# Kernel optimization log

Hardware: AMD Instinct MI355X
Metric: run time of the kernel (lower is better)

## Reference

```python
import jax, jax.numpy as jnp
import numpy as np

N_NODES = 10000
N_EDGES = 160000
BATCH = 16
F_IN = 32          # NODE_EMBED_SIZE
HEADS = 4
HDIM = 4
HC = HEADS * HDIM  # 16
N_LAYERS = 4
OBS_DIM = 100
NUM_OUT = 30
HID = 128
POOL_OUT = 15


def setup_inputs() -> dict:
    key = jax.random.key(0)
    ks = jax.random.split(key, 26)
    s = 0.1
    d = {}
    d["x"] = jax.random.normal(ks[0], (BATCH, N_NODES, F_IN), jnp.float32)
    d["obs"] = jax.random.normal(ks[1], (BATCH, OBS_DIM), jnp.float32)
    d["src"] = jax.random.randint(ks[2], (N_EDGES,), 0, N_NODES)
    d["dst"] = jax.random.randint(ks[3], (N_EDGES,), 0, N_NODES)
    # layer 0 (in=F_IN), layers 1..3 (in=HC) GATv2 params
    d["W0l"] = jax.random.normal(ks[4], (F_IN, HC)) * s
    d["W0r"] = jax.random.normal(ks[5], (F_IN, HC)) * s
    d["b0l"] = jnp.zeros((HC,), jnp.float32)
    d["b0r"] = jnp.zeros((HC,), jnp.float32)
    d["Wl"] = jax.random.normal(ks[6], (N_LAYERS - 1, HC, HC)) * s
    d["Wr"] = jax.random.normal(ks[7], (N_LAYERS - 1, HC, HC)) * s
    d["bl"] = jnp.zeros((N_LAYERS - 1, HC), jnp.float32)
    d["br"] = jnp.zeros((N_LAYERS - 1, HC), jnp.float32)
    d["att"] = jax.random.normal(ks[8], (N_LAYERS, HEADS, HDIM)) * s
    d["bias"] = jnp.zeros((N_LAYERS, HC), jnp.float32)
    # mean-pool aggregator projection to 15
    d["Wp"] = jax.random.normal(ks[9], (HC, POOL_OUT)) * s
    d["bp"] = jnp.zeros((POOL_OUT,), jnp.float32)
    # hybrid policy head: cat([feat15, obs100]) -> 128 -> 128 -> num_outputs
    d["W1"] = jax.random.normal(ks[10], (POOL_OUT + OBS_DIM, HID)) * s
    d["b1"] = jnp.zeros((HID,), jnp.float32)
    d["W2"] = jax.random.normal(ks[11], (HID, HID)) * s
    d["b2"] = jnp.zeros((HID,), jnp.float32)
    d["W3"] = jax.random.normal(ks[12], (HID, NUM_OUT)) * s
    d["b3"] = jnp.zeros((NUM_OUT,), jnp.float32)
    return d


def _gatv2_layer(x, src, dst, Wl, Wr, bl, br, att, bias):
    # x: [B,N,F]; src/dst: [E'] (self loops included); att: [H,C]
    B, N, _ = x.shape
    H, C = att.shape
    xl = (x @ Wl + bl).reshape(B, N, H, C)  # source transform
    xr = (x @ Wr + br).reshape(B, N, H, C)  # target transform
    z = jax.nn.leaky_relu(xl[:, src] + xr[:, dst], negative_slope=0.2)  # [B,E,H,C]
    e = jnp.einsum('behc,hc->ebh', z, att)  # [E,B,H] edge-major for segment ops
    m = jax.lax.stop_gradient(jax.ops.segment_max(e, dst, num_segments=N))
    m = jnp.where(jnp.isfinite(m), m, 0.0)
    ex = jnp.exp(e - m[dst])
    ssum = jax.ops.segment_sum(ex, dst, num_segments=N)
    alpha = ex / (ssum[dst] + 1e-16)  # softmax over incoming edges of dst
    msg = xl[:, src] * jnp.transpose(alpha, (1, 0, 2))[..., None]  # [B,E,H,C]
    out = jax.ops.segment_sum(jnp.transpose(msg, (1, 0, 2, 3)), dst, num_segments=N)
    return jnp.transpose(out, (1, 0, 2, 3)).reshape(B, N, H * C) + bias


def reference(x, obs, src, dst, W0l, W0r, b0l, b0r, Wl, Wr, bl, br, att, bias,
              Wp, bp, W1, b1, W2, b2, W3, b3):
    N = x.shape[1]
    loop = jnp.arange(N, dtype=src.dtype)  # PyG add_self_loops=True
    src_f = jnp.concatenate([src, loop])
    dst_f = jnp.concatenate([dst, loop])
    h = _gatv2_layer(x, src_f, dst_f, W0l, W0r, b0l, b0r, att[0], bias[0])
    for l in range(N_LAYERS - 1):
        h = _gatv2_layer(h, src_f, dst_f, Wl[l], Wr[l], bl[l], br[l], att[l + 1], bias[l + 1])
    feat = h.mean(axis=1) @ Wp + bp  # mean-pool aggregator -> [B,15]
    z1 = jnp.tanh(jnp.concatenate([feat, obs], axis=1) @ W1 + b1)
    z2 = jnp.tanh(z1 @ W2 + b2)
    return z2 @ W3 + b3  # logits [B, NUM_OUT]
```

## Files before the change

### kernel.cpp

```cpp
#include <hip/hip_runtime.h>
#include <hip/hip_fp16.h>
#include <cstdint>
#include <cstddef>

#define NN   10000
#define NE   160000
#define NB   16
#define FIN  32
#define HC   16
#define NH   4
#define HD   4
#define OBSD 100
#define NOUT 30
#define HIDD 128
#define PO   15
#define BCAP 64
#define NBUCKET 64

typedef float floatx2 __attribute__((ext_vector_type(2)));

__device__ inline uint32_t pack_fp8x4(float a, float b, float c, float d) {
    int p = __builtin_amdgcn_cvt_pk_fp8_f32(a, b, 0, false);
    p = __builtin_amdgcn_cvt_pk_fp8_f32(c, d, p, true);
    return (uint32_t)p;
}

__global__ void k_build_xform0(const int* __restrict__ src, const int* __restrict__ dst,
                               int* __restrict__ cnt, int* __restrict__ bucket,
                               const float* __restrict__ x,
                               const float* __restrict__ Wlg, const float* __restrict__ Wrg,
                               const float* __restrict__ blg, const float* __restrict__ brg,
                               uint32_t* __restrict__ xl, float* __restrict__ xr) {
    int bid = blockIdx.x;
    if (bid < 625) {
        int e = bid * 256 + threadIdx.x;
        if (e < NE) {
            int d = dst[e];
            int p = atomicAdd(&cnt[d], 1);
            if (p < BCAP) bucket[(size_t)d * BCAP + p] = src[e];
        }
        return;
    }
    __shared__ float sWl[FIN * HC], sWr[FIN * HC], sbl[HC], sbr[HC];
    for (int i = threadIdx.x; i < FIN * HC; i += 256) { sWl[i] = Wlg[i]; sWr[i] = Wrg[i]; }
    if (threadIdx.x < HC) { sbl[threadIdx.x] = blg[threadIdx.x]; sbr[threadIdx.x] = brg[threadIdx.x]; }
    __syncthreads();
    int local = bid - 625;
    int b = local / 40;
    int n = (local % 40) * 256 + threadIdx.x;
    if (n >= NN) return;
    const float* xp = x + ((size_t)b * NN + n) * FIN;
    float row[FIN];
#pragma unroll
    for (int f = 0; f < FIN; f++) row[f] = xp[f];
    float al[HC], ar[HC];
#pragma unroll
    for (int c = 0; c < HC; c++) { al[c] = sbl[c]; ar[c] = sbr[c]; }
#pragma unroll
    for (int f = 0; f < FIN; f++) {
        float v = row[f];
#pragma unroll
        for (int c = 0; c < HC; c++) {
            al[c] = fmaf(v, sWl[f * HC + c], al[c]);
            ar[c] = fmaf(v, sWr[f * HC + c], ar[c]);
        }
    }
    uint32_t* xlo = xl + ((size_t)n * NB + b) * 4;
    float*    xro = xr + ((size_t)n * NB + b) * HC;
#pragma unroll
    for (int hh = 0; hh < 4; hh++)
        xlo[hh] = pack_fp8x4(al[hh * 4 + 0], al[hh * 4 + 1], al[hh * 4 + 2], al[hh * 4 + 3]);
#pragma unroll
    for (int c = 0; c < HC; c++) xro[c] = ar[c];
}

__device__ inline float4 shfl_xor4(float4 v, int m) {
    float4 r;
    r.x = __shfl_xor(v.x, m, 64);
    r.y = __shfl_xor(v.y, m, 64);
    r.z = __shfl_xor(v.z, m, 64);
    r.w = __shfl_xor(v.w, m, 64);
    return r;
}

template <int MODE>
__global__ __launch_bounds__(256, 4)
void k_edge_f(const uint32_t* __restrict__ xl, const float* __restrict__ xr,
              const int* __restrict__ cntg, const int* __restrict__ bucket,
              const float* __restrict__ attg, const float* __restrict__ biasg,
              const float* __restrict__ Wln, const float* __restrict__ Wrn,
              const float* __restrict__ bln, const float* __restrict__ brn,
              uint32_t* __restrict__ xl_o, float* __restrict__ xr_o,
              float* __restrict__ pool_part) {
    __shared__ float sWl[HC * HC], sWr[HC * HC], sbl[HC], sbr[HC];
    if (MODE == 1) {
        int t = threadIdx.x;
        sWl[t] = Wln[t]; sWr[t] = Wrn[t];
        if (t < HC) { sbl[t] = bln[t]; sbr[t] = brn[t]; }
        __syncthreads();
    }
    int wave = (blockIdx.x * blockDim.x + threadIdx.x) >> 6;
    int lane = threadIdx.x & 63;
    const int n = wave;
    const int h = lane & 3;
    const float4 a4 = *(const float4*)(attg + h * HD);
    const float4 bias4 = *(const float4*)(biasg + h * HD);
    const float4 xr4 = *(const float4*)(xr + (size_t)n * (NB * HC) + lane * 4);
    const int cnt = __builtin_amdgcn_readfirstlane(cntg[n]);
    float4 acc = make_float4(0.f, 0.f, 0.f, 0.f);
    float ssum = 0.f;

#define EDGE_BODY(RAW, M)                                                     \
    {                                                                         \
        floatx2 f0 = __builtin_amdgcn_cvt_pk_f32_fp8((int)(RAW), false);      \
        floatx2 f1 = __builtin_amdgcn_cvt_pk_f32_fp8((int)(RAW), true);       \
        float z0 = f0.x + xr4.x; z0 = fmaxf(z0, 0.2f * z0);                   \
        float z1 = f0.y + xr4.y; z1 = fmaxf(z1, 0.2f * z1);                   \
        float z2 = f1.x + xr4.z; z2 = fmaxf(z2, 0.2f * z2);                   \
        float z3 = f1.y + xr4.w; z3 = fmaxf(z3, 0.2f * z3);                   \
        float e = fmaf(z3, a4.w, fmaf(z2, a4.z, fmaf(z1, a4.y, z0 * a4.x)));  \
        float ex = (M) * __expf(e);                                           \
        ssum += ex;                                                           \
        acc.x = fmaf(ex, f0.x, acc.x);                                        \
        acc.y = fmaf(ex, f0.y, acc.y);                                        \
        acc.z = fmaf(ex, f1.x, acc.z);                                        \
        acc.w = fmaf(ex, f1.y, acc.w);                                        \
    }
#define GATHER(S) xl[(size_t)(S) * 64 + lane]

    {
        const uint32_t r = GATHER(n);
        EDGE_BODY(r, 1.0f);
    }
    if (cnt > 0) {
        const int* brow = bucket + (size_t)n * BCAP;
        int li = lane < cnt ? lane : cnt - 1;
        int vidx = brow[li];
        for (int i = 0; i < cnt; i += 16) {
            uint32_t r[16];
#pragma unroll
            for (int u = 0; u < 16; u++) {
                int e = i + u;
                int ec = e < cnt ? e : cnt - 1;
                int s = __builtin_amdgcn_readlane(vidx, ec);
                r[u] = GATHER(s);
            }
#pragma unroll
            for (int u = 0; u < 16; u++) {
                float m = (i + u < cnt) ? 1.0f : 0.0f;
                EDGE_BODY(r[u], m);
            }
        }
    }
#undef GATHER
#undef EDGE_BODY

    float inv = 1.0f / (ssum + 1e-16f);
    float4 o;
    o.x = fmaf(acc.x, inv, bias4.x);
    o.y = fmaf(acc.y, inv, bias4.y);
    o.z = fmaf(acc.z, inv, bias4.z);
    o.w = fmaf(acc.w, inv, bias4.w);

    if (MODE == 1) {
        float accl[4], accr[4];
#pragma unroll
        for (int cj = 0; cj < 4; cj++) {
            accl[cj] = sbl[h * 4 + cj];
            accr[cj] = sbr[h * 4 + cj];
        }
#pragma unroll
        for (int m = 0; m < 4; m++) {
            float4 vals = (m == 0) ? o : shfl_xor4(o, m);
            int fbase = ((h ^ m) << 2);
            float vv[4] = {vals.x, vals.y, vals.z, vals.w};
#pragma unroll
            for (int j = 0; j < 4; j++) {
                const float4 wl = *(const float4*)&sWl[(fbase + j) * HC + (h << 2)];
                const float4 wr = *(const float4*)&sWr[(fbase + j) * HC + (h << 2)];
                float v = vv[j];
                accl[0] = fmaf(v, wl.x, accl[0]);
                accl[1] = fmaf(v, wl.y, accl[1]);
                accl[2] = fmaf(v, wl.z, accl[2]);
                accl[3] = fmaf(v, wl.w, accl[3]);
                accr[0] = fmaf(v, wr.x, accr[0]);
                accr[1] = fmaf(v, wr.y, accr[1]);
                accr[2] = fmaf(v, wr.z, accr[2]);
                accr[3] = fmaf(v, wr.w, accr[3]);
            }
        }
        xl_o[(size_t)n * 64 + lane] = pack_fp8x4(accl[0], accl[1], accl[2], accl[3]);
        *(float4*)(xr_o + (size_t)n * (NB * HC) + lane * 4) =
            make_float4(accr[0], accr[1], accr[2], accr[3]);
    } else {
        __shared__ float sRed[256 * 4];
        int tid = threadIdx.x;
        *(float4*)&sRed[tid * 4] = o;
        __syncthreads();
        if (tid < 64) {
            float4 s0 = *(const float4*)&sRed[tid * 4];
            float4 s1 = *(const float4*)&sRed[(64 + tid) * 4];
            float4 s2 = *(const float4*)&sRed[(128 + tid) * 4];
            float4 s3 = *(const float4*)&sRed[(192 + tid) * 4];
            float* dp = pool_part + (blockIdx.x & (NBUCKET - 1)) * 256 + tid * 4;
            atomicAdd(dp + 0, s0.x + s1.x + s2.x + s3.x);
            atomicAdd(dp + 1, s0.y + s1.y + s2.y + s3.y);
            atomicAdd(dp + 2, s0.z + s1.z + s2.z + s3.z);
            atomicAdd(dp + 3, s0.w + s1.w + s2.w + s3.w);
        }
    }
}

__global__ void k_head(const float* __restrict__ pool_part, const float* __restrict__ obs,
                       const float* __restrict__ Wp, const float* __restrict__ bp,
                       const float* __restrict__ W1, const float* __restrict__ b1,
                       const float* __restrict__ W2, const float* __restrict__ b2,
                       const float* __restrict__ W3, const float* __restrict__ b3,
                       float* __restrict__ out) {
    const int b = blockIdx.x;
    const int t = threadIdx.x;
    __shared__ float sPool[HC];
    __shared__ float sIn[PO + OBSD];
    __shared__ float s1[HIDD], s2[HIDD];
    if (t < HC) {
        float ps = 0.f;
        for (int p = 0; p < NBUCKET; p++) ps += pool_part[p * 256 + b * HC + t];
        sPool[t] = ps * (1.0f / NN);
    }
    for (int k = t; k < OBSD; k += 128) sIn[PO + k] = obs[b * OBSD + k];
    __syncthreads();
    if (t < PO) {
        float acc = bp[t];
#pragma unroll
        for (int c = 0; c < HC; c++) acc = fmaf(sPool[c], Wp[c * PO + t], acc);
        sIn[t] = acc;
    }
    __syncthreads();
    {
        float acc = b1[t];
        for (int k = 0; k < PO + OBSD; k++) acc = fmaf(sIn[k], W1[k * HIDD + t], acc);
        s1[t] = tanhf(acc);
    }
    __syncthreads();
    {
        float acc = b2[t];
        for (int k = 0; k < HIDD; k++) acc = fmaf(s1[k], W2[k * HIDD + t], acc);
        s2[t] = tanhf(acc);
    }
    __syncthreads();
    if (t < NOUT) {
        float acc = b3[t];
        for (int k = 0; k < HIDD; k++) acc = fmaf(s2[k], W3[k * NOUT + t], acc);
        out[b * NOUT + t] = acc;
    }
}

extern "C" void kernel_launch(void* const* d_in, const int* in_sizes, int n_in,
                              void* d_out, int out_size, void* d_ws, size_t ws_size,
                              hipStream_t stream) {
    const float* x    = (const float*)d_in[0];
    const float* obs  = (const float*)d_in[1];
    const int*   src  = (const int*)d_in[2];
    const int*   dst  = (const int*)d_in[3];
    const float* W0l  = (const float*)d_in[4];
    const float* W0r  = (const float*)d_in[5];
    const float* b0l  = (const float*)d_in[6];
    const float* b0r  = (const float*)d_in[7];
    const float* Wl   = (const float*)d_in[8];
    const float* Wr   = (const float*)d_in[9];
    const float* bl   = (const float*)d_in[10];
    const float* br   = (const float*)d_in[11];
    const float* att  = (const float*)d_in[12];
    const float* bias = (const float*)d_in[13];
    const float* Wp   = (const float*)d_in[14];
    const float* bp   = (const float*)d_in[15];
    const float* W1   = (const float*)d_in[16];
    const float* b1   = (const float*)d_in[17];
    const float* W2   = (const float*)d_in[18];
    const float* b2   = (const float*)d_in[19];
    const float* W3   = (const float*)d_in[20];
    const float* b3   = (const float*)d_in[21];
    float* out = (float*)d_out;

    size_t off = 0;
    auto take = [&](size_t bytes) -> void* {
        void* p = (char*)d_ws + off;
        off += (bytes + 255) & ~(size_t)255;
        return p;
    };
    int*      cnt       = (int*)take(NN * sizeof(int));
    float*    pool_part = (float*)take(NBUCKET * 256 * sizeof(float));
    int*      bucket    = (int*)take((size_t)NN * BCAP * sizeof(int));
    uint32_t* xlA       = (uint32_t*)take((size_t)NN * 64 * sizeof(uint32_t));
    float*    xrA       = (float*)take((size_t)NN * NB * HC * sizeof(float));
    uint32_t* xlB       = (uint32_t*)take((size_t)NN * 64 * sizeof(uint32_t));
    float*    xrB       = (float*)take((size_t)NN * NB * HC * sizeof(float));

    size_t zspan = (size_t)((char*)(pool_part + NBUCKET * 256) - (char*)cnt);
    hipMemsetAsync(cnt, 0, zspan, stream);

    k_build_xform0<<<625 + 40 * NB, 256, 0, stream>>>(src, dst, cnt, bucket,
                                                      x, W0l, W0r, b0l, b0r, xlA, xrA);

    const int EG = (NN * 64) / 256;
    k_edge_f<1><<<EG, 256, 0, stream>>>(xlA, xrA, cnt, bucket,
                                        att + 0 * 16, bias + 0 * 16,
                                        Wl + 0 * 256, Wr + 0 * 256, bl + 0 * 16, br + 0 * 16,
                                        xlB, xrB, nullptr);
    k_edge_f<1><<<EG, 256, 0, stream>>>(xlB, xrB, cnt, bucket,
                                        att + 1 * 16, bias + 1 * 16,
                                        Wl + 1 * 256, Wr + 1 * 256, bl + 1 * 16, br + 1 * 16,
                                        xlA, xrA, nullptr);
    k_edge_f<1><<<EG, 256, 0, stream>>>(xlA, xrA, cnt, bucket,
                                        att + 2 * 16, bias + 2 * 16,
                                        Wl + 2 * 256, Wr + 2 * 256, bl + 2 * 16, br + 2 * 16,
                                        xlB, xrB, nullptr);
    k_edge_f<2><<<EG, 256, 0, stream>>>(xlB, xrB, cnt, bucket,
                                        att + 3 * 16, bias + 3 * 16,
                                        nullptr, nullptr, nullptr, nullptr,
                                        nullptr, nullptr, pool_part);

    k_head<<<NB, HIDD, 0, stream>>>(pool_part, obs, Wp, bp, W1, b1, W2, b2, W3, b3, out);
}
```

Baseline: 131.3 us.

## Store xr in fp16 and fuse policy head into last edge kernel

The xr target-transform buffers change from fp32 to fp16, halving their write and read traffic in every layer. The separate k_head launch is removed: the last edge kernel counts finished blocks with an atomic, and the last block reduces the pool partials and runs the MLP head for all 16 batches itself. The number of pool-partial buckets is halved and the bucket count is clamped to BCAP. This trades one launch and some memory traffic for fp16 precision loss and a head computed serially by a single block.

```diff
diff --git a/kernel.cpp b/kernel.cpp
--- a/kernel.cpp
+++ b/kernel.cpp
@@ -15,7 +15,8 @@
 #define HIDD 128
 #define PO   15
 #define BCAP 64
-#define NBUCKET 64
+#define NBUCKET 32
+#define EG   2500
 
 typedef float floatx2 __attribute__((ext_vector_type(2)));
 
@@ -23,6 +24,15 @@
     int p = __builtin_amdgcn_cvt_pk_fp8_f32(a, b, 0, false);
     p = __builtin_amdgcn_cvt_pk_fp8_f32(c, d, p, true);
     return (uint32_t)p;
+}
+
+__device__ inline float4 shfl_xor4(float4 v, int m) {
+    float4 r;
+    r.x = __shfl_xor(v.x, m, 64);
+    r.y = __shfl_xor(v.y, m, 64);
+    r.z = __shfl_xor(v.z, m, 64);
+    r.w = __shfl_xor(v.w, m, 64);
+    return r;
 }
 
 __global__ void k_build_xform0(const int* __restrict__ src, const int* __restrict__ dst,
@@ -30,7 +40,7 @@
                                const float* __restrict__ x,
                                const float* __restrict__ Wlg, const float* __restrict__ Wrg,
                                const float* __restrict__ blg, const float* __restrict__ brg,
-                               uint32_t* __restrict__ xl, float* __restrict__ xr) {
+                               uint32_t* __restrict__ xl, __half* __restrict__ xr) {
     int bid = blockIdx.x;
     if (bid < 625) {
         int e = bid * 256 + threadIdx.x;
@@ -66,47 +76,53 @@
         }
     }
     uint32_t* xlo = xl + ((size_t)n * NB + b) * 4;
-    float*    xro = xr + ((size_t)n * NB + b) * HC;
+    __half2*  xro = (__half2*)(xr + ((size_t)n * NB + b) * HC);
 #pragma unroll
     for (int hh = 0; hh < 4; hh++)
         xlo[hh] = pack_fp8x4(al[hh * 4 + 0], al[hh * 4 + 1], al[hh * 4 + 2], al[hh * 4 + 3]);
 #pragma unroll
-    for (int c = 0; c < HC; c++) xro[c] = ar[c];
-}
-
-__device__ inline float4 shfl_xor4(float4 v, int m) {
-    float4 r;
-    r.x = __shfl_xor(v.x, m, 64);
-    r.y = __shfl_xor(v.y, m, 64);
-    r.z = __shfl_xor(v.z, m, 64);
-    r.w = __shfl_xor(v.w, m, 64);
-    return r;
+    for (int c = 0; c < HC; c += 2) xro[c >> 1] = __floats2half2_rn(ar[c], ar[c + 1]);
 }
 
 template <int MODE>
 __global__ __launch_bounds__(256, 4)
-void k_edge_f(const uint32_t* __restrict__ xl, const float* __restrict__ xr,
+void k_edge_f(const uint32_t* __restrict__ xl, const __half* __restrict__ xr,
               const int* __restrict__ cntg, const int* __restrict__ bucket,
               const float* __restrict__ attg, const float* __restrict__ biasg,
               const float* __restrict__ Wln, const float* __restrict__ Wrn,
               const float* __restrict__ bln, const float* __restrict__ brn,
-              uint32_t* __restrict__ xl_o, float* __restrict__ xr_o,
-              float* __restrict__ pool_part) {
-    __shared__ float sWl[HC * HC], sWr[HC * HC], sbl[HC], sbr[HC];
+              uint32_t* __restrict__ xl_o, __half* __restrict__ xr_o,
+              float* __restrict__ pool_part, int* __restrict__ done,
+              const float* __restrict__ obs,
+              const float* __restrict__ Wp, const float* __restrict__ bp,
+              const float* __restrict__ W1, const float* __restrict__ b1,
+              const float* __restrict__ W2, const float* __restrict__ b2,
+              const float* __restrict__ W3, const float* __restrict__ b3,
+              float* __restrict__ out) {
+    __shared__ float smem[MODE == 2 ? 6208 : 544];
     if (MODE == 1) {
         int t = threadIdx.x;
-        sWl[t] = Wln[t]; sWr[t] = Wrn[t];
-        if (t < HC) { sbl[t] = bln[t]; sbr[t] = brn[t]; }
-        __syncthreads();
-    }
-    int wave = (blockIdx.x * blockDim.x + threadIdx.x) >> 6;
-    int lane = threadIdx.x & 63;
+        smem[t] = Wln[t];
+        smem[256 + t] = Wrn[t];
+        if (t < HC) { smem[512 + t] = bln[t]; smem[528 + t] = brn[t]; }
+        __syncthreads();
+    }
+    const int tid  = threadIdx.x;
+    const int wave = (blockIdx.x * 256 + tid) >> 6;
+    const int lane = tid & 63;
     const int n = wave;
     const int h = lane & 3;
     const float4 a4 = *(const float4*)(attg + h * HD);
     const float4 bias4 = *(const float4*)(biasg + h * HD);
-    const float4 xr4 = *(const float4*)(xr + (size_t)n * (NB * HC) + lane * 4);
-    const int cnt = __builtin_amdgcn_readfirstlane(cntg[n]);
+    float4 xr4;
+    {
+        const uint2 xrr = *(const uint2*)(xr + (size_t)n * (NB * HC) + lane * 4);
+        float2 p0 = __half22float2(*(const __half2*)&xrr.x);
+        float2 p1 = __half22float2(*(const __half2*)&xrr.y);
+        xr4 = make_float4(p0.x, p0.y, p1.x, p1.y);
+    }
+    int cnt = __builtin_amdgcn_readfirstlane(cntg[n]);
+    cnt = cnt < BCAP ? cnt : BCAP;
     float4 acc = make_float4(0.f, 0.f, 0.f, 0.f);
     float ssum = 0.f;
 
@@ -128,10 +144,7 @@
     }
 #define GATHER(S) xl[(size_t)(S) * 64 + lane]
 
-    {
-        const uint32_t r = GATHER(n);
-        EDGE_BODY(r, 1.0f);
-    }
+    { const uint32_t r = GATHER(n); EDGE_BODY(r, 1.0f); }
     if (cnt > 0) {
         const int* brow = bucket + (size_t)n * BCAP;
         int li = lane < cnt ? lane : cnt - 1;
@@ -166,8 +179,8 @@
         float accl[4], accr[4];
 #pragma unroll
         for (int cj = 0; cj < 4; cj++) {
-            accl[cj] = sbl[h * 4 + cj];
-            accr[cj] = sbr[h * 4 + cj];
+            accl[cj] = smem[512 + h * 4 + cj];
+            accr[cj] = smem[528 + h * 4 + cj];
         }
 #pragma unroll
         for (int m = 0; m < 4; m++) {
@@ -176,8 +189,8 @@
             float vv[4] = {vals.x, vals.y, vals.z, vals.w};
 #pragma unroll
             for (int j = 0; j < 4; j++) {
-                const float4 wl = *(const float4*)&sWl[(fbase + j) * HC + (h << 2)];
-                const float4 wr = *(const float4*)&sWr[(fbase + j) * HC + (h << 2)];
+                const float4 wl = *(const float4*)&smem[(fbase + j) * HC + (h << 2)];
+                const float4 wr = *(const float4*)&smem[256 + (fbase + j) * HC + (h << 2)];
                 float v = vv[j];
                 accl[0] = fmaf(v, wl.x, accl[0]);
                 accl[1] = fmaf(v, wl.y, accl[1]);
@@ -190,68 +203,80 @@
             }
         }
         xl_o[(size_t)n * 64 + lane] = pack_fp8x4(accl[0], accl[1], accl[2], accl[3]);
-        *(float4*)(xr_o + (size_t)n * (NB * HC) + lane * 4) =
-            make_float4(accr[0], accr[1], accr[2], accr[3]);
+        __half2* xro = (__half2*)(xr_o + (size_t)n * (NB * HC) + lane * 4);
+        xro[0] = __floats2half2_rn(accr[0], accr[1]);
+        xro[1] = __floats2half2_rn(accr[2], accr[3]);
     } else {
-        __shared__ float sRed[256 * 4];
-        int tid = threadIdx.x;
+        float* sRed = smem;
         *(float4*)&sRed[tid * 4] = o;
         __syncthreads();
         if (tid < 64) {
             float4 s0 = *(const float4*)&sRed[tid * 4];
-            float4 s1 = *(const float4*)&sRed[(64 + tid) * 4];
-            float4 s2 = *(const float4*)&sRed[(128 + tid) * 4];
-            float4 s3 = *(const float4*)&sRed[(192 + tid) * 4];
+            float4 s1v = *(const float4*)&sRed[(64 + tid) * 4];
+            float4 s2v = *(const float4*)&sRed[(128 + tid) * 4];
+            float4 s3v = *(const float4*)&sRed[(192 + tid) * 4];
             float* dp = pool_part + (blockIdx.x & (NBUCKET - 1)) * 256 + tid * 4;
-            atomicAdd(dp + 0, s0.x + s1.x + s2.x + s3.x);
-            atomicAdd(dp + 1, s0.y + s1.y + s2.y + s3.y);
-            atomicAdd(dp + 2, s0.z + s1.z + s2.z + s3.z);
-            atomicAdd(dp + 3, s0.w + s1.w + s2.w + s3.w);
-        }
-    }
-}
-
-__global__ void k_head(const float* __restrict__ pool_part, const float* __restrict__ obs,
-                       const float* __restrict__ Wp, const float* __restrict__ bp,
-                       const float* __restrict__ W1, const float* __restrict__ b1,
-                       const float* __restrict__ W2, const float* __restrict__ b2,
-                       const float* __restrict__ W3, const float* __restrict__ b3,
-                       float* __restrict__ out) {
-    const int b = blockIdx.x;
-    const int t = threadIdx.x;
-    __shared__ float sPool[HC];
-    __shared__ float sIn[PO + OBSD];
-    __shared__ float s1[HIDD], s2[HIDD];
-    if (t < HC) {
-        float ps = 0.f;
-        for (int p = 0; p < NBUCKET; p++) ps += pool_part[p * 256 + b * HC + t];
-        sPool[t] = ps * (1.0f / NN);
-    }
-    for (int k = t; k < OBSD; k += 128) sIn[PO + k] = obs[b * OBSD + k];
-    __syncthreads();
-    if (t < PO) {
-        float acc = bp[t];
-#pragma unroll
-        for (int c = 0; c < HC; c++) acc = fmaf(sPool[c], Wp[c * PO + t], acc);
-        sIn[t] = acc;
-    }
-    __syncthreads();
-    {
-        float acc = b1[t];
-        for (int k = 0; k < PO + OBSD; k++) acc = fmaf(sIn[k], W1[k * HIDD + t], acc);
-        s1[t] = tanhf(acc);
-    }
-    __syncthreads();
-    {
-        float acc = b2[t];
-        for (int k = 0; k < HIDD; k++) acc = fmaf(s1[k], W2[k * HIDD + t], acc);
-        s2[t] = tanhf(acc);
-    }
-    __syncthreads();
-    if (t < NOUT) {
-        float acc = b3[t];
-        for (int k = 0; k < HIDD; k++) acc = fmaf(s2[k], W3[k * NOUT + t], acc);
-        out[b * NOUT + t] = acc;
+            atomicAdd(dp + 0, s0.x + s1v.x + s2v.x + s3v.x);
+            atomicAdd(dp + 1, s0.y + s1v.y + s2v.y + s3v.y);
+            atomicAdd(dp + 2, s0.z + s1v.z + s2v.z + s3v.z);
+            atomicAdd(dp + 3, s0.w + s1v.w + s2v.w + s3v.w);
+        }
+        __syncthreads();
+        __shared__ int lastFlag;
+        if (tid == 0) {
+            int t = __hip_atomic_fetch_add(done, 1, __ATOMIC_ACQ_REL,
+                                           __HIP_MEMORY_SCOPE_AGENT);
+            lastFlag = (t == EG - 1) ? 1 : 0;
+        }
+        __syncthreads();
+        if (!lastFlag) return;
+
+        float* sPool = smem;
+        float* sIn   = smem + 256;
+        float* s1a   = smem + 2112;
+        float* s2a   = smem + 4160;
+        {
+            int b = tid >> 4, c = tid & 15;
+            float ps = 0.f;
+            for (int q = 0; q < NBUCKET; q++)
+                ps += __hip_atomic_load(&pool_part[q * 256 + b * HC + c],
+                                        __ATOMIC_RELAXED, __HIP_MEMORY_SCOPE_AGENT);
+            sPool[tid] = ps * (1.0f / NN);
+        }
+        __syncthreads();
+        for (int k = tid; k < NB * (PO + OBSD); k += 256) {
+            int b = k / (PO + OBSD), j = k - b * (PO + OBSD);
+            float v;
+            if (j < PO) {
+                v = bp[j];
+#pragma unroll
+                for (int c = 0; c < HC; c++) v = fmaf(sPool[b * HC + c], Wp[c * PO + j], v);
+            } else {
+                v = obs[b * OBSD + (j - PO)];
+            }
+            sIn[b * 116 + j] = v;
+        }
+        __syncthreads();
+        for (int k = tid; k < NB * HIDD; k += 256) {
+            int b = k >> 7, t = k & 127;
+            float acc2 = b1[t];
+            for (int j = 0; j < PO + OBSD; j++) acc2 = fmaf(sIn[b * 116 + j], W1[j * HIDD + t], acc2);
+            s1a[k] = tanhf(acc2);
+        }
+        __syncthreads();
+        for (int k = tid; k < NB * HIDD; k += 256) {
+            int b = k >> 7, t = k & 127;
+            float acc2 = b2[t];
+            for (int j = 0; j < HIDD; j++) acc2 = fmaf(s1a[b * 128 + j], W2[j * HIDD + t], acc2);
+            s2a[k] = tanhf(acc2);
+        }
+        __syncthreads();
+        for (int k = tid; k < NB * NOUT; k += 256) {
+            int b = k / NOUT, t = k - b * NOUT;
+            float acc2 = b3[t];
+            for (int j = 0; j < HIDD; j++) acc2 = fmaf(s2a[b * 128 + j], W3[j * NOUT + t], acc2);
+            out[k] = acc2;
+        }
     }
 }
 
@@ -284,41 +309,46 @@
 
     size_t off = 0;
     auto take = [&](size_t bytes) -> void* {
-        void* p = (char*)d_ws + off;
+        void* ptr = (char*)d_ws + off;
         off += (bytes + 255) & ~(size_t)255;
-        return p;
+        return ptr;
     };
+    int*      done      = (int*)take(64 * sizeof(int));
     int*      cnt       = (int*)take(NN * sizeof(int));
     float*    pool_part = (float*)take(NBUCKET * 256 * sizeof(float));
     int*      bucket    = (int*)take((size_t)NN * BCAP * sizeof(int));
     uint32_t* xlA       = (uint32_t*)take((size_t)NN * 64 * sizeof(uint32_t));
-    float*    xrA       = (float*)take((size_t)NN * NB * HC * sizeof(float));
+    __half*   xrA       = (__half*)take((size_t)NN * NB * HC * sizeof(__half));
     uint32_t* xlB       = (uint32_t*)take((size_t)NN * 64 * sizeof(uint32_t));
-    float*    xrB       = (float*)take((size_t)NN * NB * HC * sizeof(float));
-
-    size_t zspan = (size_t)((char*)(pool_part + NBUCKET * 256) - (char*)cnt);
-    hipMemsetAsync(cnt, 0, zspan, stream);
+    __half*   xrB       = (__half*)take((size_t)NN * NB * HC * sizeof(__half));
+
+    size_t zspan = (size_t)((char*)(pool_part + NBUCKET * 256) - (char*)done);
+    hipMemsetAsync(done, 0, zspan, stream);
 
     k_build_xform0<<<625 + 40 * NB, 256, 0, stream>>>(src, dst, cnt, bucket,
                                                       x, W0l, W0r, b0l, b0r, xlA, xrA);
 
-    const int EG = (NN * 64) / 256;
     k_edge_f<1><<<EG, 256, 0, stream>>>(xlA, xrA, cnt, bucket,
                                         att + 0 * 16, bias + 0 * 16,
                                         Wl + 0 * 256, Wr + 0 * 256, bl + 0 * 16, br + 0 * 16,
-                                        xlB, xrB, nullptr);
+                                        xlB, xrB, nullptr, nullptr,
+                                        nullptr, nullptr, nullptr, nullptr, nullptr,
+                                        nullptr, nullptr, nullptr, nullptr, nullptr);
     k_edge_f<1><<<EG, 256, 0, stream>>>(xlB, xrB, cnt, bucket,
                                         att + 1 * 16, bias + 1 * 16,
                                         Wl + 1 * 256, Wr + 1 * 256, bl + 1 * 16, br + 1 * 16,
-                                        xlA, xrA, nullptr);
+                                        xlA, xrA, nullptr, nullptr,
+                                        nullptr, nullptr, nullptr, nullptr, nullptr,
+                                        nullptr, nullptr, nullptr, nullptr, nullptr);
     k_edge_f<1><<<EG, 256, 0, stream>>>(xlA, xrA, cnt, bucket,
                                         att + 2 * 16, bias + 2 * 16,
                                         Wl + 2 * 256, Wr + 2 * 256, bl + 2 * 16, br + 2 * 16,
-                                        xlB, xrB, nullptr);
+                                        xlB, xrB, nullptr, nullptr,
+                                        nullptr, nullptr, nullptr, nullptr, nullptr,
+                                        nullptr, nullptr, nullptr, nullptr, nullptr);
     k_edge_f<2><<<EG, 256, 0, stream>>>(xlB, xrB, cnt, bucket,
                                         att + 3 * 16, bias + 3 * 16,
                                         nullptr, nullptr, nullptr, nullptr,
-                                        nullptr, nullptr, pool_part);
-
-    k_head<<<NB, HIDD, 0, stream>>>(pool_part, obs, Wp, bp, W1, b1, W2, b2, W3, b3, out);
-}
+                                        nullptr, nullptr, pool_part, done,
+                                        obs, Wp, bp, W1, b1, W2, b2, W3, b3, out);
+}
```

Result: slower. 206.2 us (+57.1%).

## Store xr in fp16 and replace pool atomics with per-block partials

Applied to the files above, without the earlier changes.

The target-side transform xr is now stored as fp16 instead of fp32, which halves its memory traffic in every edge layer and lowers precision. The final layer no longer does atomicAdd into 64 buckets; each block writes its own 256-float partial, and the head kernel, now 256 threads, reduces all 2500 partials. This removes atomic contention and the memset of the pool buffer, but adds a serial reduction inside the small head kernel. The edge count is also clamped to BCAP, and shared memory is merged into a single array.

```diff
diff --git a/kernel.cpp b/kernel.cpp
--- a/kernel.cpp
+++ b/kernel.cpp
@@ -15,7 +15,7 @@
 #define HIDD 128
 #define PO   15
 #define BCAP 64
-#define NBUCKET 64
+#define EG   2500
 
 typedef float floatx2 __attribute__((ext_vector_type(2)));
 
@@ -23,6 +23,15 @@
     int p = __builtin_amdgcn_cvt_pk_fp8_f32(a, b, 0, false);
     p = __builtin_amdgcn_cvt_pk_fp8_f32(c, d, p, true);
     return (uint32_t)p;
+}
+
+__device__ inline float4 shfl_xor4(float4 v, int m) {
+    float4 r;
+    r.x = __shfl_xor(v.x, m, 64);
+    r.y = __shfl_xor(v.y, m, 64);
+    r.z = __shfl_xor(v.z, m, 64);
+    r.w = __shfl_xor(v.w, m, 64);
+    return r;
 }
 
 __global__ void k_build_xform0(const int* __restrict__ src, const int* __restrict__ dst,
@@ -30,7 +39,7 @@
                                const float* __restrict__ x,
                                const float* __restrict__ Wlg, const float* __restrict__ Wrg,
                                const float* __restrict__ blg, const float* __restrict__ brg,
-                               uint32_t* __restrict__ xl, float* __restrict__ xr) {
+                               uint32_t* __restrict__ xl, __half* __restrict__ xr) {
     int bid = blockIdx.x;
     if (bid < 625) {
         int e = bid * 256 + threadIdx.x;
@@ -66,47 +75,47 @@
         }
     }
     uint32_t* xlo = xl + ((size_t)n * NB + b) * 4;
-    float*    xro = xr + ((size_t)n * NB + b) * HC;
+    __half2*  xro = (__half2*)(xr + ((size_t)n * NB + b) * HC);
 #pragma unroll
     for (int hh = 0; hh < 4; hh++)
         xlo[hh] = pack_fp8x4(al[hh * 4 + 0], al[hh * 4 + 1], al[hh * 4 + 2], al[hh * 4 + 3]);
 #pragma unroll
-    for (int c = 0; c < HC; c++) xro[c] = ar[c];
-}
-
-__device__ inline float4 shfl_xor4(float4 v, int m) {
-    float4 r;
-    r.x = __shfl_xor(v.x, m, 64);
-    r.y = __shfl_xor(v.y, m, 64);
-    r.z = __shfl_xor(v.z, m, 64);
-    r.w = __shfl_xor(v.w, m, 64);
-    return r;
+    for (int c = 0; c < HC; c += 2) xro[c >> 1] = __floats2half2_rn(ar[c], ar[c + 1]);
 }
 
 template <int MODE>
 __global__ __launch_bounds__(256, 4)
-void k_edge_f(const uint32_t* __restrict__ xl, const float* __restrict__ xr,
+void k_edge_f(const uint32_t* __restrict__ xl, const __half* __restrict__ xr,
               const int* __restrict__ cntg, const int* __restrict__ bucket,
               const float* __restrict__ attg, const float* __restrict__ biasg,
               const float* __restrict__ Wln, const float* __restrict__ Wrn,
               const float* __restrict__ bln, const float* __restrict__ brn,
-              uint32_t* __restrict__ xl_o, float* __restrict__ xr_o,
+              uint32_t* __restrict__ xl_o, __half* __restrict__ xr_o,
               float* __restrict__ pool_part) {
-    __shared__ float sWl[HC * HC], sWr[HC * HC], sbl[HC], sbr[HC];
+    __shared__ float smem[MODE == 2 ? 1024 : 544];
     if (MODE == 1) {
         int t = threadIdx.x;
-        sWl[t] = Wln[t]; sWr[t] = Wrn[t];
-        if (t < HC) { sbl[t] = bln[t]; sbr[t] = brn[t]; }
+        smem[t] = Wln[t];
+        smem[256 + t] = Wrn[t];
+        if (t < HC) { smem[512 + t] = bln[t]; smem[528 + t] = brn[t]; }
         __syncthreads();
     }
-    int wave = (blockIdx.x * blockDim.x + threadIdx.x) >> 6;
-    int lane = threadIdx.x & 63;
+    const int tid  = threadIdx.x;
+    const int wave = (blockIdx.x * 256 + tid) >> 6;
+    const int lane = tid & 63;
     const int n = wave;
     const int h = lane & 3;
     const float4 a4 = *(const float4*)(attg + h * HD);
     const float4 bias4 = *(const float4*)(biasg + h * HD);
-    const float4 xr4 = *(const float4*)(xr + (size_t)n * (NB * HC) + lane * 4);
-    const int cnt = __builtin_amdgcn_readfirstlane(cntg[n]);
+    float4 xr4;
+    {
+        const uint2 xrr = *(const uint2*)(xr + (size_t)n * (NB * HC) + lane * 4);
+        float2 p0 = __half22float2(*(const __half2*)&xrr.x);
+        float2 p1 = __half22float2(*(const __half2*)&xrr.y);
+        xr4 = make_float4(p0.x, p0.y, p1.x, p1.y);
+    }
+    int cnt = __builtin_amdgcn_readfirstlane(cntg[n]);
+    cnt = cnt < BCAP ? cnt : BCAP;
     float4 acc = make_float4(0.f, 0.f, 0.f, 0.f);
     float ssum = 0.f;
 
@@ -128,10 +137,7 @@
     }
 #define GATHER(S) xl[(size_t)(S) * 64 + lane]
 
-    {
-        const uint32_t r = GATHER(n);
-        EDGE_BODY(r, 1.0f);
-    }
+    { const uint32_t r = GATHER(n); EDGE_BODY(r, 1.0f); }
     if (cnt > 0) {
         const int* brow = bucket + (size_t)n * BCAP;
         int li = lane < cnt ? lane : cnt - 1;
@@ -166,8 +172,8 @@
         float accl[4], accr[4];
 #pragma unroll
         for (int cj = 0; cj < 4; cj++) {
-            accl[cj] = sbl[h * 4 + cj];
-            accr[cj] = sbr[h * 4 + cj];
+            accl[cj] = smem[512 + h * 4 + cj];
+            accr[cj] = smem[528 + h * 4 + cj];
         }
 #pragma unroll
         for (int m = 0; m < 4; m++) {
@@ -176,8 +182,8 @@
             float vv[4] = {vals.x, vals.y, vals.z, vals.w};
 #pragma unroll
             for (int j = 0; j < 4; j++) {
-                const float4 wl = *(const float4*)&sWl[(fbase + j) * HC + (h << 2)];
-                const float4 wr = *(const float4*)&sWr[(fbase + j) * HC + (h << 2)];
+                const float4 wl = *(const float4*)&smem[(fbase + j) * HC + (h << 2)];
+                const float4 wr = *(const float4*)&smem[256 + (fbase + j) * HC + (h << 2)];
                 float v = vv[j];
                 accl[0] = fmaf(v, wl.x, accl[0]);
                 accl[1] = fmaf(v, wl.y, accl[1]);
@@ -190,23 +196,22 @@
             }
         }
         xl_o[(size_t)n * 64 + lane] = pack_fp8x4(accl[0], accl[1], accl[2], accl[3]);
-        *(float4*)(xr_o + (size_t)n * (NB * HC) + lane * 4) =
-            make_float4(accr[0], accr[1], accr[2], accr[3]);
+        __half2* xro = (__half2*)(xr_o + (size_t)n * (NB * HC) + lane * 4);
+        xro[0] = __floats2half2_rn(accr[0], accr[1]);
+        xro[1] = __floats2half2_rn(accr[2], accr[3]);
     } else {
-        __shared__ float sRed[256 * 4];
-        int tid = threadIdx.x;
-        *(float4*)&sRed[tid * 4] = o;
+        *(float4*)&smem[tid * 4] = o;
         __syncthreads();
         if (tid < 64) {
-            float4 s0 = *(const float4*)&sRed[tid * 4];
-            float4 s1 = *(const float4*)&sRed[(64 + tid) * 4];
-            float4 s2 = *(const float4*)&sRed[(128 + tid) * 4];
-            float4 s3 = *(const float4*)&sRed[(192 + tid) * 4];
-            float* dp = pool_part + (blockIdx.x & (NBUCKET - 1)) * 256 + tid * 4;
-            atomicAdd(dp + 0, s0.x + s1.x + s2.x + s3.x);
-            atomicAdd(dp + 1, s0.y + s1.y + s2.y + s3.y);
-            atomicAdd(dp + 2, s0.z + s1.z + s2.z + s3.z);
-            atomicAdd(dp + 3, s0.w + s1.w + s2.w + s3.w);
+            float4 s0 = *(const float4*)&smem[tid * 4];
+            float4 s1v = *(const float4*)&smem[(64 + tid) * 4];
+            float4 s2v = *(const float4*)&smem[(128 + tid) * 4];
+            float4 s3v = *(const float4*)&smem[(192 + tid) * 4];
+            *(float4*)(pool_part + (size_t)blockIdx.x * 256 + tid * 4) =
+                make_float4(s0.x + s1v.x + s2v.x + s3v.x,
+                            s0.y + s1v.y + s2v.y + s3v.y,
+                            s0.z + s1v.z + s2v.z + s3v.z,
+                            s0.w + s1v.w + s2v.w + s3v.w);
         }
     }
 }
@@ -219,15 +224,25 @@
                        float* __restrict__ out) {
     const int b = blockIdx.x;
     const int t = threadIdx.x;
+    __shared__ float sPart[256];
     __shared__ float sPool[HC];
     __shared__ float sIn[PO + OBSD];
     __shared__ float s1[HIDD], s2[HIDD];
+    {
+        int c = t & 15, chunk = t >> 4;
+        float ps = 0.f;
+        for (int p = chunk; p < EG; p += 16)
+            ps += pool_part[(size_t)p * 256 + b * HC + c];
+        sPart[t] = ps;
+    }
+    __syncthreads();
     if (t < HC) {
         float ps = 0.f;
-        for (int p = 0; p < NBUCKET; p++) ps += pool_part[p * 256 + b * HC + t];
+#pragma unroll
+        for (int chunk = 0; chunk < 16; chunk++) ps += sPart[chunk * 16 + t];
         sPool[t] = ps * (1.0f / NN);
     }
-    for (int k = t; k < OBSD; k += 128) sIn[PO + k] = obs[b * OBSD + k];
+    for (int k = t; k < OBSD; k += 256) sIn[PO + k] = obs[b * OBSD + k];
     __syncthreads();
     if (t < PO) {
         float acc = bp[t];
@@ -236,13 +251,13 @@
         sIn[t] = acc;
     }
     __syncthreads();
-    {
+    if (t < HIDD) {
         float acc = b1[t];
         for (int k = 0; k < PO + OBSD; k++) acc = fmaf(sIn[k], W1[k * HIDD + t], acc);
         s1[t] = tanhf(acc);
     }
     __syncthreads();
-    {
+    if (t < HIDD) {
         float acc = b2[t];
         for (int k = 0; k < HIDD; k++) acc = fmaf(s1[k], W2[k * HIDD + t], acc);
         s2[t] = tanhf(acc);
@@ -284,25 +299,23 @@
 
     size_t off = 0;
     auto take = [&](size_t bytes) -> void* {
-        void* p = (char*)d_ws + off;
+        void* ptr = (char*)d_ws + off;
         off += (bytes + 255) & ~(size_t)255;
-        return p;
+        return ptr;
     };
     int*      cnt       = (int*)take(NN * sizeof(int));
-    float*    pool_part = (float*)take(NBUCKET * 256 * sizeof(float));
+    float*    pool_part = (float*)take((size_t)EG * 256 * sizeof(float));
     int*      bucket    = (int*)take((size_t)NN * BCAP * sizeof(int));
     uint32_t* xlA       = (uint32_t*)take((size_t)NN * 64 * sizeof(uint32_t));
-    float*    xrA       = (float*)take((size_t)NN * NB * HC * sizeof(float));
+    __half*   xrA       = (__half*)take((size_t)NN * NB * HC * sizeof(__half));
     uint32_t* xlB       = (uint32_t*)take((size_t)NN * 64 * sizeof(uint32_t));
-    float*    xrB       = (float*)take((size_t)NN * NB * HC * sizeof(float));
-
-    size_t zspan = (size_t)((char*)(pool_part + NBUCKET * 256) - (char*)cnt);
-    hipMemsetAsync(cnt, 0, zspan, stream);
+    __half*   xrB       = (__half*)take((size_t)NN * NB * HC * sizeof(__half));
+
+    hipMemsetAsync(cnt, 0, NN * sizeof(int), stream);
 
     k_build_xform0<<<625 + 40 * NB, 256, 0, stream>>>(src, dst, cnt, bucket,
                                                       x, W0l, W0r, b0l, b0r, xlA, xrA);
 
-    const int EG = (NN * 64) / 256;
     k_edge_f<1><<<EG, 256, 0, stream>>>(xlA, xrA, cnt, bucket,
                                         att + 0 * 16, bias + 0 * 16,
                                         Wl + 0 * 256, Wr + 0 * 256, bl + 0 * 16, br + 0 * 16,
@@ -320,5 +333,5 @@
                                         nullptr, nullptr, nullptr, nullptr,
                                         nullptr, nullptr, pool_part);
 
-    k_head<<<NB, HIDD, 0, stream>>>(pool_part, obs, Wp, bp, W1, b1, W2, b2, W3, b3, out);
-}
+    k_head<<<NB, 256, 0, stream>>>(pool_part, obs, Wp, bp, W1, b1, W2, b2, W3, b3, out);
+}
```

Result: slower. 171.4 us (+30.6%).
